# Optimization experiments

Measured on AMD Instinct MI355X. Metric: run time of the kernel, lower is better.

The kernel has to match this reference:

```python
import jax, jax.numpy as jnp
import numpy as np

B, C, H, W = 16, 64, 1024, 16  # requires C*W == H per the module's implicit view/matmul constraint
C8 = C // 8


def setup_inputs() -> dict:
    key = jax.random.key(0)
    ks = jax.random.split(key, 7)
    s_in = 1.0 / np.sqrt(C)
    return {
        "x": jax.random.normal(ks[0], (B, C, H, W), dtype=jnp.float32),
        "Wq": jax.random.normal(ks[1], (C8, C), dtype=jnp.float32) * s_in,
        "bq": jax.random.normal(ks[2], (C8,), dtype=jnp.float32) * 0.01,
        "Wk": jax.random.normal(ks[3], (C8, C), dtype=jnp.float32) * s_in,
        "bk": jax.random.normal(ks[4], (C8,), dtype=jnp.float32) * 0.01,
        "Wv": jax.random.normal(ks[5], (C, C), dtype=jnp.float32) * s_in,
        "bv": jax.random.normal(ks[6], (C,), dtype=jnp.float32) * 0.01,
    }


def conv1x1(x, w, b):
    # 1x1 conv == per-pixel channel mixing: [B,C,H,W] x [O,C] -> [B,O,H,W]
    return jnp.einsum("bchw,oc->bohw", x, w) + b[None, :, None, None]


def reference(x, Wq, bq, Wk, bk, Wv, bv):
    b, c, h, w = x.shape
    q = conv1x1(x, Wq, bq)  # [B, C/8, H, W]
    k = conv1x1(x, Wk, bk)  # [B, C/8, H, W]
    v = conv1x1(x, Wv, bv)  # [B, C, H, W]
    # Faithful to torch .view(B, -1, H): row-major reshape, NOT a transpose.
    qf = jnp.swapaxes(q.reshape(b, -1, h), 1, 2)  # [B, H, C8*W]
    kf = k.reshape(b, -1, h)                      # [B, C8*W, H]
    vf = v.reshape(b, -1, h)                      # [B, C*W, H] (C*W == H)
    scores = jax.nn.softmax(jnp.matmul(qf, kf), axis=-1)  # [B, H, H]
    attended = jnp.matmul(scores, vf)             # [B, H, H]
    attended = attended.reshape(v.shape)          # [B, C, H, W]
    return x + attended
```

## Files before the change

### kernel.cpp

```cpp
#include <hip/hip_runtime.h>
#include <stdint.h>

typedef uint32_t u32;
typedef __attribute__((ext_vector_type(4))) float f32x4;
typedef __attribute__((ext_vector_type(8))) short short8;

#define NBATCH 16
#define NPIX   16384
#define NPB    1048576

__device__ __forceinline__ ushort f2bf(float f) {
  u32 b = __builtin_bit_cast(u32, f);
  return (ushort)((b + 0x7FFFu + ((b >> 16) & 1u)) >> 16);
}
__device__ __forceinline__ float bf2f(ushort h) {
  return __builtin_bit_cast(float, (u32)h << 16);
}

__device__ __forceinline__ void gload16(const void* g, void* l) {
  __builtin_amdgcn_global_load_lds(
      (const __attribute__((address_space(1))) u32*)g,
      (__attribute__((address_space(3))) u32*)l,
      16, 0, 0);
}

__global__ void prep_w2(const float* __restrict__ Wq, const float* __restrict__ bq,
                        const float* __restrict__ Wk, const float* __restrict__ bk,
                        const float* __restrict__ Wv, const float* __restrict__ bv,
                        ushort* __restrict__ Wpk, float* __restrict__ bpk)
{
  int gid = blockIdx.x * 256 + threadIdx.x;
  if (gid < 12288) {
    int m = gid >> 7, kk = gid & 127;
    int ch = kk & 63;
    ushort outv = 0;
    if (m < 8) {
      float wv = Wq[m * 64 + ch];
      ushort h = f2bf(wv);
      outv = (kk < 64) ? h : f2bf(wv - bf2f(h));
    } else if (m < 16) {
      float wv = Wk[(m - 8) * 64 + ch];
      ushort h = f2bf(wv);
      outv = (kk < 64) ? h : f2bf(wv - bf2f(h));
    } else if (m < 80) {
      outv = (kk < 64) ? f2bf(Wv[(m - 16) * 64 + ch]) : (ushort)0;
    }
    Wpk[gid] = outv;
  } else if (gid < 12368) {
    int o = gid - 12288;
    bpk[o] = (o < 8) ? bq[o] : (o < 16 ? bk[o - 8] : bv[o - 16]);
  }
}

__global__ __launch_bounds__(256) void proj10(
    const float* __restrict__ x, const ushort* __restrict__ Wpk,
    const float* __restrict__ bpk,
    ushort* __restrict__ Qt2, ushort* __restrict__ Kt2,
    ushort* __restrict__ Vt)
{
  __shared__ __align__(16) char smem[32768];
  float* xs = (float*)smem;
  int t = threadIdx.x;
  int w = t >> 6, lane = t & 63;
  int l15 = lane & 15, l4 = lane >> 4;

  int g = blockIdx.x;
  int lin = (g & 7) * 256 + (g >> 3);
  int b = lin >> 7;
  int l0 = (lin & 127) << 3;
  const float* xb = x + (size_t)b * NPB + l0;

  #pragma unroll
  for (int it = 0; it < 8; ++it) {
    int f0 = (it * 4 + w) * 64;
    int f = f0 + lane;
    int ch = f >> 5, r2 = f & 31, tc = r2 >> 1, half = r2 & 1;
    gload16(xb + (size_t)ch * NPIX + tc * 1024 + half * 4, xs + f0 * 4);
  }

  const uint4* Wp4 = (const uint4*)Wpk;
  uint4 Afrag[12];
  #pragma unroll
  for (int kc = 0; kc < 4; ++kc)
    Afrag[kc] = Wp4[l15 * 16 + kc * 4 + l4];
  #pragma unroll
  for (int mt = 1; mt < 5; ++mt)
    #pragma unroll
    for (int kc = 0; kc < 2; ++kc)
      Afrag[2 + mt * 2 + kc] = Wp4[(mt * 16 + l15) * 16 + kc * 4 + l4];

  f32x4 acc[5][2];
  #pragma unroll
  for (int mt = 0; mt < 5; ++mt) {
    f32x4 bv4;
    #pragma unroll
    for (int r = 0; r < 4; ++r) bv4[r] = bpk[mt * 16 + l4 * 4 + r];
    acc[mt][0] = bv4; acc[mt][1] = bv4;
  }

  __syncthreads();

  #pragma unroll
  for (int i = 0; i < 2; ++i) {
    int px = (w * 2 + i) * 16 + l15;
    u32 xr[16];
    #pragma unroll
    for (int kc = 0; kc < 2; ++kc)
      #pragma unroll
      for (int j = 0; j < 8; ++j)
        xr[kc * 8 + j] = ((const u32*)xs)[(kc * 32 + l4 * 8 + j) * 128 + px];
    uint4 bxh[2], bxl[2];
    #pragma unroll
    for (int kc = 0; kc < 2; ++kc)
      #pragma unroll
      for (int p = 0; p < 4; ++p) {
        u32 a = xr[kc * 8 + 2 * p], c = xr[kc * 8 + 2 * p + 1];
        ((u32*)&bxh[kc])[p] = (a >> 16) | (c & 0xFFFF0000u);
        float fa = __builtin_bit_cast(float, a) -
                   __builtin_bit_cast(float, a & 0xFFFF0000u);
        float fc = __builtin_bit_cast(float, c) -
                   __builtin_bit_cast(float, c & 0xFFFF0000u);
        u32 la = __builtin_bit_cast(u32, fa), lc = __builtin_bit_cast(u32, fc);
        ((u32*)&bxl[kc])[p] = (la >> 16) | (lc & 0xFFFF0000u);
      }
    short8 h0 = __builtin_bit_cast(short8, bxh[0]);
    short8 h1 = __builtin_bit_cast(short8, bxh[1]);
    short8 s0 = __builtin_bit_cast(short8, bxl[0]);
    short8 s1 = __builtin_bit_cast(short8, bxl[1]);
    acc[0][i] = __builtin_amdgcn_mfma_f32_16x16x32_bf16(
        __builtin_bit_cast(short8, Afrag[0]), h0, acc[0][i], 0, 0, 0);
    acc[0][i] = __builtin_amdgcn_mfma_f32_16x16x32_bf16(
        __builtin_bit_cast(short8, Afrag[1]), h1, acc[0][i], 0, 0, 0);
    acc[0][i] = __builtin_amdgcn_mfma_f32_16x16x32_bf16(
        __builtin_bit_cast(short8, Afrag[0]), s0, acc[0][i], 0, 0, 0);
    acc[0][i] = __builtin_amdgcn_mfma_f32_16x16x32_bf16(
        __builtin_bit_cast(short8, Afrag[1]), s1, acc[0][i], 0, 0, 0);
    acc[0][i] = __builtin_amdgcn_mfma_f32_16x16x32_bf16(
        __builtin_bit_cast(short8, Afrag[2]), h0, acc[0][i], 0, 0, 0);
    acc[0][i] = __builtin_amdgcn_mfma_f32_16x16x32_bf16(
        __builtin_bit_cast(short8, Afrag[3]), h1, acc[0][i], 0, 0, 0);
    #pragma unroll
    for (int mt = 1; mt < 5; ++mt) {
      acc[mt][i] = __builtin_amdgcn_mfma_f32_16x16x32_bf16(
          __builtin_bit_cast(short8, Afrag[2 + mt * 2]), h0, acc[mt][i], 0, 0, 0);
      acc[mt][i] = __builtin_amdgcn_mfma_f32_16x16x32_bf16(
          __builtin_bit_cast(short8, Afrag[3 + mt * 2]), h1, acc[mt][i], 0, 0, 0);
    }
  }
  __syncthreads();

  float*  qkl = (float*)smem;
  ushort* vl  = (ushort*)(smem + 16 * 132 * 4);
  #pragma unroll
  for (int i = 0; i < 2; ++i) {
    int px = (w * 2 + i) * 16 + l15;
    #pragma unroll
    for (int r = 0; r < 4; ++r)
      qkl[(l4 * 4 + r) * 132 + px] = acc[0][i][r];
    #pragma unroll
    for (int mt = 1; mt < 5; ++mt)
      #pragma unroll
      for (int r = 0; r < 4; ++r)
        vl[((mt - 1) * 16 + l4 * 4 + r) * 136 + px] = f2bf(acc[mt][i][r]);
  }
  __syncthreads();

  if (t < 128) {
    int l = t >> 4, tcc = t & 15;
    size_t lrow = (size_t)b * 1024 + l0 + l;
    int px = tcc * 8 + l;

    union { ushort s[8]; uint4 v; } qh, ql, kh, kl;
    #pragma unroll
    for (int o = 0; o < 8; ++o) {
      float qv = qkl[o * 132 + px];
      ushort h = f2bf(qv);
      qh.s[o] = h; ql.s[o] = f2bf(qv - bf2f(h));
      float kv = qkl[(8 + o) * 132 + px];
      h = f2bf(kv);
      kh.s[o] = h; kl.s[o] = f2bf(kv - bf2f(h));
    }
    ushort* qrow = Qt2 + lrow * 384 + tcc * 8;
    *(uint4*)qrow         = qh.v;
    *(uint4*)(qrow + 128) = ql.v;
    *(uint4*)(qrow + 256) = qh.v;
    ushort* krow = Kt2 + lrow * 384 + tcc * 8;
    *(uint4*)krow         = kh.v;
    *(uint4*)(krow + 128) = kh.v;
    *(uint4*)(krow + 256) = kl.v;

    ushort* vrow = Vt + lrow * 1024;
    #pragma unroll
    for (int it = 0; it < 4; ++it) {
      int c2 = (it << 4) + tcc;
      union { ushort s[16]; uint4 q[2]; } ov;
      #pragma unroll
      for (int tt = 0; tt < 16; ++tt)
        ov.s[tt] = vl[c2 * 136 + tt * 8 + l];
      *(uint4*)(vrow + c2 * 16)     = ov.q[0];
      *(uint4*)(vrow + c2 * 16 + 8) = ov.q[1];
    }
  }
}

template<int KTOT, bool ADDX>
__global__ __launch_bounds__(256) void gemm_nt(
    const ushort* __restrict__ A, int lda,
    const ushort* __restrict__ B, int ldb,
    float* __restrict__ C, const float* __restrict__ X)
{
  __shared__ ushort Asm[2][128 * 64];
  __shared__ ushort Bsm[2][128 * 64];
  int t = threadIdx.x;

  int g = blockIdx.x;
  int lin = (g & 7) * 128 + (g >> 3);
  int bz = lin >> 6;
  int by = (lin >> 3) & 7;
  int bx = lin & 7;
  int m0 = by << 7, n0 = bx << 7;

  const ushort* Ab = A + (size_t)bz * 1024 * lda;
  const ushort* Bb = B + (size_t)bz * 1024 * ldb;
  int wid = t >> 6, lane = t & 63;
  int wm = wid >> 1, wn = wid & 1;

  int swc = (t & 7) ^ ((t >> 3) & 7);
  const ushort* pa = Ab + (size_t)(m0 + (t >> 3)) * lda + swc * 8;
  const ushort* pb = Bb + (size_t)(n0 + (t >> 3)) * ldb + swc * 8;
  int wb = (t >> 6) * 512;

  f32x4 acc[4][4] = {};
  constexpr int NT = KTOT / 64;

  #pragma unroll
  for (int i = 0; i < 4; ++i)
    gload16(pa + (size_t)i * 32 * lda, Asm[0] + wb + i * 2048);
  #pragma unroll
  for (int i = 0; i < 4; ++i)
    gload16(pb + (size_t)i * 32 * ldb, Bsm[0] + wb + i * 2048);
  asm volatile("s_waitcnt vmcnt(0)" ::: "memory");
  __builtin_amdgcn_s_barrier();

  #pragma unroll 2
  for (int it = 0; it < NT; ++it) {
    int cur = it & 1;
    if (it + 1 < NT) {
      int k0 = (it + 1) * 64;
      #pragma unroll
      for (int i = 0; i < 4; ++i)
        gload16(pa + (size_t)i * 32 * lda + k0, Asm[cur ^ 1] + wb + i * 2048);
      #pragma unroll
      for (int i = 0; i < 4; ++i)
        gload16(pb + (size_t)i * 32 * ldb + k0, Bsm[cur ^ 1] + wb + i * 2048);
    }
    #pragma unroll
    for (int kk = 0; kk < 2; ++kk) {
      short8 af[4], bfr[4];
      #pragma unroll
      for (int mi = 0; mi < 4; ++mi) {
        int rr = (wm << 6) + (mi << 4) + (lane & 15);
        af[mi] = __builtin_bit_cast(short8,
            ((const uint4*)Asm[cur])[rr * 8 + ((kk * 4 + (lane >> 4)) ^ (rr & 7))]);
      }
      #pragma unroll
      for (int ni = 0; ni < 4; ++ni) {
        int rr = (wn << 6) + (ni << 4) + (lane & 15);
        bfr[ni] = __builtin_bit_cast(short8,
            ((const uint4*)Bsm[cur])[rr * 8 + ((kk * 4 + (lane >> 4)) ^ (rr & 7))]);
      }
      #pragma unroll
      for (int mi = 0; mi < 4; ++mi)
        #pragma unroll
        for (int ni = 0; ni < 4; ++ni)
          acc[mi][ni] = __builtin_amdgcn_mfma_f32_16x16x32_bf16(
              af[mi], bfr[ni], acc[mi][ni], 0, 0, 0);
    }
    asm volatile("s_waitcnt vmcnt(0)" ::: "memory");
    __builtin_amdgcn_s_barrier();
  }

  #pragma unroll
  for (int mi = 0; mi < 4; ++mi) {
    int rbase = m0 + (wm << 6) + (mi << 4) + ((lane >> 4) << 2);
    #pragma unroll
    for (int ni = 0; ni < 4; ++ni) {
      int col = n0 + (wn << 6) + (ni << 4) + (lane & 15);
      f32x4 v = acc[mi][ni];
      #pragma unroll
      for (int rr = 0; rr < 4; ++rr) {
        size_t idx = ((size_t)bz * 1024 + rbase + rr) * 1024 + col;
        if (ADDX) C[idx] = v[rr] + X[idx];
        else      C[idx] = v[rr];
      }
    }
  }
}

__global__ __launch_bounds__(256) void softmax_rows(float* __restrict__ S)
{
  size_t rowi = blockIdx.x;
  float* srow = S + rowi * 1024;
  int t = threadIdx.x;
  float4 v = ((const float4*)srow)[t];
  float m = fmaxf(fmaxf(v.x, v.y), fmaxf(v.z, v.w));
  #pragma unroll
  for (int off = 32; off > 0; off >>= 1) m = fmaxf(m, __shfl_xor(m, off));
  __shared__ float red[8];
  int wid = t >> 6, lane = t & 63;
  if (lane == 0) red[wid] = m;
  __syncthreads();
  m = fmaxf(fmaxf(red[0], red[1]), fmaxf(red[2], red[3]));
  float e0 = __expf(v.x - m), e1 = __expf(v.y - m);
  float e2 = __expf(v.z - m), e3 = __expf(v.w - m);
  float s = e0 + e1 + e2 + e3;
  #pragma unroll
  for (int off = 32; off > 0; off >>= 1) s += __shfl_xor(s, off);
  if (lane == 0) red[4 + wid] = s;
  __syncthreads();
  s = red[4] + red[5] + red[6] + red[7];
  float inv = 1.0f / s;
  union { ushort h[4]; uint2 q; } pk;
  pk.h[0] = f2bf(e0 * inv); pk.h[1] = f2bf(e1 * inv);
  pk.h[2] = f2bf(e2 * inv); pk.h[3] = f2bf(e3 * inv);
  ((uint2*)srow)[t] = pk.q;
}

extern "C" void kernel_launch(void* const* d_in, const int* in_sizes, int n_in,
                              void* d_out, int out_size, void* d_ws, size_t ws_size,
                              hipStream_t stream) {
  const float* x  = (const float*)d_in[0];
  const float* Wq = (const float*)d_in[1];
  const float* bq = (const float*)d_in[2];
  const float* Wk = (const float*)d_in[3];
  const float* bk = (const float*)d_in[4];
  const float* Wv = (const float*)d_in[5];
  const float* bv = (const float*)d_in[6];
  float* out = (float*)d_out;

  char* wsb = (char*)d_ws;
  ushort* Qt2 = (ushort*)wsb;
  ushort* Kt2 = (ushort*)(wsb + 12582912);
  ushort* Vt  = (ushort*)(wsb + 25165824);
  float*  S   = (float*)(wsb + 58720256);
  ushort* Wpk = (ushort*)(wsb + 92274688);
  float*  bpk = (float*)(wsb + 92274688 + 24576);

  prep_w2<<<49, 256, 0, stream>>>(Wq, bq, Wk, bk, Wv, bv, Wpk, bpk);
  proj10<<<2048, 256, 0, stream>>>(x, Wpk, bpk, Qt2, Kt2, Vt);
  gemm_nt<384, false><<<1024, 256, 0, stream>>>(Qt2, 384, Kt2, 384, S, nullptr);
  softmax_rows<<<16384, 256, 0, stream>>>(S);
  gemm_nt<1024, true><<<1024, 256, 0, stream>>>((const ushort*)S, 2048, Vt, 1024, out, x);
}
```

Baseline: 139.5 us.

## Enlarge GEMM tiles to 256x256 with 512-thread blocks

Replaces the 128x128 GEMM kernel with a 256x256 tile version using 8 waves per block, each computing a 128x64 sub-tile. The goal is more data reuse per LDS load and less global traffic per output, with a quarter as many blocks. In exchange, LDS use reaches 128KB per block and each thread holds twice the accumulator registers, which can lower occupancy. With only 256 blocks on a 256-CU device, load balance and latency hiding may suffer.

```diff
diff --git a/kernel.cpp b/kernel.cpp
--- a/kernel.cpp
+++ b/kernel.cpp
@@ -204,73 +204,76 @@
 }
 
 template<int KTOT, bool ADDX>
-__global__ __launch_bounds__(256) void gemm_nt(
+__global__ __launch_bounds__(512, 2) void gemm256(
     const ushort* __restrict__ A, int lda,
     const ushort* __restrict__ B, int ldb,
     float* __restrict__ C, const float* __restrict__ X)
 {
-  __shared__ ushort Asm[2][128 * 64];
-  __shared__ ushort Bsm[2][128 * 64];
+  __shared__ ushort AB[2][2][16384];
   int t = threadIdx.x;
 
   int g = blockIdx.x;
-  int lin = (g & 7) * 128 + (g >> 3);
-  int bz = lin >> 6;
-  int by = (lin >> 3) & 7;
-  int bx = lin & 7;
-  int m0 = by << 7, n0 = bx << 7;
+  int lin = (g & 7) * 32 + (g >> 3);
+  int bz = lin >> 4;
+  int by = (lin >> 2) & 3;
+  int bx = lin & 3;
+  int m0 = by << 8, n0 = bx << 8;
 
   const ushort* Ab = A + (size_t)bz * 1024 * lda;
   const ushort* Bb = B + (size_t)bz * 1024 * ldb;
-  int wid = t >> 6, lane = t & 63;
-  int wm = wid >> 1, wn = wid & 1;
+  int w = t >> 6, lane = t & 63;
+  int wm = w >> 2, wn = w & 3;
+  int l15 = lane & 15, l4 = lane >> 4;
 
   int swc = (t & 7) ^ ((t >> 3) & 7);
   const ushort* pa = Ab + (size_t)(m0 + (t >> 3)) * lda + swc * 8;
   const ushort* pb = Bb + (size_t)(n0 + (t >> 3)) * ldb + swc * 8;
-  int wb = (t >> 6) * 512;
-
-  f32x4 acc[4][4] = {};
+  int wb = w * 512;
+
+  f32x4 acc[8][4] = {};
   constexpr int NT = KTOT / 64;
 
   #pragma unroll
   for (int i = 0; i < 4; ++i)
-    gload16(pa + (size_t)i * 32 * lda, Asm[0] + wb + i * 2048);
+    gload16(pa + (size_t)i * 64 * lda, AB[0][0] + i * 4096 + wb);
   #pragma unroll
   for (int i = 0; i < 4; ++i)
-    gload16(pb + (size_t)i * 32 * ldb, Bsm[0] + wb + i * 2048);
+    gload16(pb + (size_t)i * 64 * ldb, AB[0][1] + i * 4096 + wb);
   asm volatile("s_waitcnt vmcnt(0)" ::: "memory");
   __builtin_amdgcn_s_barrier();
 
-  #pragma unroll 2
   for (int it = 0; it < NT; ++it) {
     int cur = it & 1;
+    const ushort* As = AB[cur][0];
+    const ushort* Bs = AB[cur][1];
     if (it + 1 < NT) {
       int k0 = (it + 1) * 64;
+      ushort* An = AB[cur ^ 1][0];
+      ushort* Bn = AB[cur ^ 1][1];
       #pragma unroll
       for (int i = 0; i < 4; ++i)
-        gload16(pa + (size_t)i * 32 * lda + k0, Asm[cur ^ 1] + wb + i * 2048);
+        gload16(pa + (size_t)i * 64 * lda + k0, An + i * 4096 + wb);
       #pragma unroll
       for (int i = 0; i < 4; ++i)
-        gload16(pb + (size_t)i * 32 * ldb + k0, Bsm[cur ^ 1] + wb + i * 2048);
+        gload16(pb + (size_t)i * 64 * ldb + k0, Bn + i * 4096 + wb);
     }
     #pragma unroll
     for (int kk = 0; kk < 2; ++kk) {
-      short8 af[4], bfr[4];
-      #pragma unroll
-      for (int mi = 0; mi < 4; ++mi) {
-        int rr = (wm << 6) + (mi << 4) + (lane & 15);
+      short8 af[8], bfr[4];
+      #pragma unroll
+      for (int mi = 0; mi < 8; ++mi) {
+        int rr = (wm << 7) + (mi << 4) + l15;
         af[mi] = __builtin_bit_cast(short8,
-            ((const uint4*)Asm[cur])[rr * 8 + ((kk * 4 + (lane >> 4)) ^ (rr & 7))]);
+            ((const uint4*)As)[rr * 8 + ((kk * 4 + l4) ^ (rr & 7))]);
       }
       #pragma unroll
       for (int ni = 0; ni < 4; ++ni) {
-        int rr = (wn << 6) + (ni << 4) + (lane & 15);
+        int rr = (wn << 6) + (ni << 4) + l15;
         bfr[ni] = __builtin_bit_cast(short8,
-            ((const uint4*)Bsm[cur])[rr * 8 + ((kk * 4 + (lane >> 4)) ^ (rr & 7))]);
+            ((const uint4*)Bs)[rr * 8 + ((kk * 4 + l4) ^ (rr & 7))]);
       }
       #pragma unroll
-      for (int mi = 0; mi < 4; ++mi)
+      for (int mi = 0; mi < 8; ++mi)
         #pragma unroll
         for (int ni = 0; ni < 4; ++ni)
           acc[mi][ni] = __builtin_amdgcn_mfma_f32_16x16x32_bf16(
@@ -281,11 +284,11 @@
   }
 
   #pragma unroll
-  for (int mi = 0; mi < 4; ++mi) {
-    int rbase = m0 + (wm << 6) + (mi << 4) + ((lane >> 4) << 2);
+  for (int mi = 0; mi < 8; ++mi) {
+    int rbase = m0 + (wm << 7) + (mi << 4) + (l4 << 2);
     #pragma unroll
     for (int ni = 0; ni < 4; ++ni) {
-      int col = n0 + (wn << 6) + (ni << 4) + (lane & 15);
+      int col = n0 + (wn << 6) + (ni << 4) + l15;
       f32x4 v = acc[mi][ni];
       #pragma unroll
       for (int rr = 0; rr < 4; ++rr) {
@@ -348,7 +351,7 @@
 
   prep_w2<<<49, 256, 0, stream>>>(Wq, bq, Wk, bk, Wv, bv, Wpk, bpk);
   proj10<<<2048, 256, 0, stream>>>(x, Wpk, bpk, Qt2, Kt2, Vt);
-  gemm_nt<384, false><<<1024, 256, 0, stream>>>(Qt2, 384, Kt2, 384, S, nullptr);
+  gemm256<384, false><<<256, 512, 0, stream>>>(Qt2, 384, Kt2, 384, S, nullptr);
   softmax_rows<<<16384, 256, 0, stream>>>(S);
-  gemm_nt<1024, true><<<1024, 256, 0, stream>>>((const ushort*)S, 2048, Vt, 1024, out, x);
-}
+  gemm256<1024, true><<<256, 512, 0, stream>>>((const ushort*)S, 2048, Vt, 1024, out, x);
+}
```

Result: faster. 128.0 us (-8.3%).
